# Optimization experiments

Measured on AMD Instinct MI355X. Metric: run time of the kernel, lower is better.

## Reference

```python
import jax, jax.numpy as jnp
import numpy as np

B = 64
D = 4096          # width of every layer
# DAG: layer k consumes concat of prior layer outputs listed here (0 = input x)
CONNECTIONS = {1: [0], 2: [0, 1], 3: [1, 2], 4: [2, 3]}


def setup_inputs() -> dict:
    key = jax.random.key(0)
    keys = iter(jax.random.split(key, 32))
    inp = {"x": jax.random.normal(next(keys), (B, D), dtype=jnp.float32)}
    for k, v in CONNECTIONS.items():
        fan_in = D * len(v)
        bound = 1.0 / np.sqrt(fan_in)
        # kaiming_uniform_(a=sqrt(5)) -> U(-sqrt(6/((1+5)*fan_in)), +) = U(-1/sqrt(fan_in), +)
        inp[f"W{k}"] = jax.random.uniform(next(keys), (D, fan_in), jnp.float32, -bound, bound)
        inp[f"b{k}"] = jax.random.uniform(next(keys), (D,), jnp.float32, -bound, bound)
        # static binary mask (buffer in torch), stored as float like MaskedLinear expects
        inp[f"M{k}"] = (jax.random.uniform(next(keys), (D, fan_in)) < 0.5).astype(jnp.float32)
    return inp


def _dag_forward(x, Ws, bs, Ms):
    layer_output = [x]
    for k, v in CONNECTIONS.items():
        inputs = jnp.concatenate([layer_output[v_] for v_ in v], axis=1)  # [B, D*len(v)]
        # masked linear: y = inputs @ (W*M)^T + b, then ReLU
        y = jnp.einsum('bi,oi->bo', inputs, Ws[k] * Ms[k]) + bs[k]
        layer_output.append(jax.nn.relu(y))
    return layer_output[-1]


def reference(x, W1, b1, M1, W2, b2, M2, W3, b3, M3, W4, b4, M4):
    Ws = {1: W1, 2: W2, 3: W3, 4: W4}
    bs = {1: b1, 2: b2, 3: b3, 4: b4}
    Ms = {1: M1, 2: M2, 3: M3, 4: M4}
    return _dag_forward(x, Ws, bs, Ms)
```

## Files before the change

kernel.cpp:

```cpp
#include <hip/hip_runtime.h>
#include <hip/hip_bf16.h>
#include <stdint.h>


typedef __attribute__((ext_vector_type(8))) short  s8v;
typedef __attribute__((ext_vector_type(4))) float  f4v;
typedef __attribute__((ext_vector_type(2))) float  f2v;
typedef __attribute__((ext_vector_type(4))) unsigned short us4v;
typedef __attribute__((ext_vector_type(2))) unsigned short us2v;

#define LDA 16384
#define MFMA16 __builtin_amdgcn_mfma_f32_16x16x32_bf16

__device__ __forceinline__ short f2bf(float f) {
  unsigned int u = __builtin_bit_cast(unsigned int, f);
  u += 0x7fffu + ((u >> 16) & 1u);
  return (short)(u >> 16);
}
__device__ __forceinline__ float bf2f(short s) {
  unsigned int u = ((unsigned int)(unsigned short)s) << 16;
  return __builtin_bit_cast(float, u);
}

__global__ void dag_splitx(const float* __restrict__ x,
                           ushort* __restrict__ xh, ushort* __restrict__ xl) {
  int idx = blockIdx.x * blockDim.x + threadIdx.x;
  int m = idx >> 10;
  int n = (idx & 1023) << 2;
  f4v v = *(const f4v*)(x + (size_t)m * 4096 + n);
  us4v h, l;
#pragma unroll
  for (int j = 0; j < 4; ++j) {
    short hh = f2bf(v[j]);
    h[j] = (unsigned short)hh;
    l[j] = (unsigned short)f2bf(v[j] - bf2f(hh));
  }
  *(us4v*)(xh + (size_t)m * LDA + n) = h;
  *(us4v*)(xl + (size_t)m * LDA + n) = l;
}

struct RA { s8v ah0, ah1, ah2, ah3, al0, al1, al2, al3; };

template <int NSUPER>
__global__ __launch_bounds__(256, 2) void dag_gemm_phaseA(
    const ushort* __restrict__ Ah,
    const ushort* __restrict__ Al,
    const float*  __restrict__ W,
    const float*  __restrict__ Mm,
    float*        __restrict__ partial,
    int K) {
  extern __shared__ float smem[];
  const int tid  = threadIdx.x;
  const int wave = tid >> 6, lane = tid & 63;
  const int l15  = lane & 15, blk = lane >> 4;
  const int n0   = blockIdx.x * 128 + wave * 32;
  const int klen = NSUPER * 64;
  const int kbeg = blockIdx.y * klen;

  float* WL = smem + wave * 4096;
  float* ML = WL + 2048;

  const int srow = lane >> 4;
  const int sc   = lane & 15;

  const ushort* ap  = Ah + (size_t)l15 * LDA + kbeg + blk * 8;
  const ushort* alp = Al + (size_t)l15 * LDA + kbeg + blk * 8;

  f4v stW[8], stM[8];
  f4v acc[4][2];
#pragma unroll
  for (int i = 0; i < 4; ++i) {
    acc[i][0] = (f4v){0.f, 0.f, 0.f, 0.f};
    acc[i][1] = (f4v){0.f, 0.f, 0.f, 0.f};
  }
  RA a0, a1;

  auto GLOAD = [&](int s) {
    const float* wb = W  + (size_t)n0 * K + kbeg + s * 64 + sc * 4;
    const float* mb = Mm + (size_t)n0 * K + kbeg + s * 64 + sc * 4;
#pragma unroll
    for (int j = 0; j < 8; ++j) {
      size_t ro = (size_t)(4 * j + srow) * K;
      stW[j] = *(const f4v*)(wb + ro);
      stM[j] = *(const f4v*)(mb + ro);
    }
  };
  auto DSWRITE = [&]() {
#pragma unroll
    for (int j = 0; j < 8; ++j) {
      int row = 4 * j + srow;
      int ci  = sc ^ (row & 15);
      *(f4v*)(WL + row * 64 + ci * 4) = stW[j];
      *(f4v*)(ML + row * 64 + ci * 4) = stM[j];
    }
  };
  auto LOADA = [&](RA& r, int ko) {
    r.ah0 = *(const s8v*)(ap  + ko);
    r.ah1 = *(const s8v*)(ap  + (size_t)16 * LDA + ko);
    r.ah2 = *(const s8v*)(ap  + (size_t)32 * LDA + ko);
    r.ah3 = *(const s8v*)(ap  + (size_t)48 * LDA + ko);
    r.al0 = *(const s8v*)(alp + ko);
    r.al1 = *(const s8v*)(alp + (size_t)16 * LDA + ko);
    r.al2 = *(const s8v*)(alp + (size_t)32 * LDA + ko);
    r.al3 = *(const s8v*)(alp + (size_t)48 * LDA + ko);
  };

  auto KSTEP = [&](int kstep, RA& ra) {
    const int cc = kstep * 8 + blk * 2;
    const int c0 = cc ^ l15, c1 = (cc + 1) ^ l15;
    const float* wr0 = WL + l15 * 64;
    const float* wr1 = WL + (l15 + 16) * 64;
    const float* mr0 = ML + l15 * 64;
    const float* mr1 = ML + (l15 + 16) * 64;
    f4v w0a = *(const f4v*)(wr0 + c0 * 4), w0b = *(const f4v*)(wr0 + c1 * 4);
    f4v w1a = *(const f4v*)(wr1 + c0 * 4), w1b = *(const f4v*)(wr1 + c1 * 4);
    f4v m0a = *(const f4v*)(mr0 + c0 * 4), m0b = *(const f4v*)(mr0 + c1 * 4);
    f4v m1a = *(const f4v*)(mr1 + c0 * 4), m1b = *(const f4v*)(mr1 + c1 * 4);

    s8v wh0, wl0, wh1, wl1;
#pragma unroll
    for (int j = 0; j < 4; ++j) {
      { float ww = w0a[j] * m0a[j]; short h = f2bf(ww);
        wh0[j]     = h; wl0[j]     = f2bf(ww - bf2f(h)); }
      { float ww = w0b[j] * m0b[j]; short h = f2bf(ww);
        wh0[j + 4] = h; wl0[j + 4] = f2bf(ww - bf2f(h)); }
      { float ww = w1a[j] * m1a[j]; short h = f2bf(ww);
        wh1[j]     = h; wl1[j]     = f2bf(ww - bf2f(h)); }
      { float ww = w1b[j] * m1b[j]; short h = f2bf(ww);
        wh1[j + 4] = h; wl1[j + 4] = f2bf(ww - bf2f(h)); }
    }
    acc[0][0] = MFMA16(ra.ah0, wh0, acc[0][0], 0, 0, 0);
    acc[0][0] = MFMA16(ra.al0, wh0, acc[0][0], 0, 0, 0);
    acc[0][0] = MFMA16(ra.ah0, wl0, acc[0][0], 0, 0, 0);
    acc[1][0] = MFMA16(ra.ah1, wh0, acc[1][0], 0, 0, 0);
    acc[1][0] = MFMA16(ra.al1, wh0, acc[1][0], 0, 0, 0);
    acc[1][0] = MFMA16(ra.ah1, wl0, acc[1][0], 0, 0, 0);
    acc[2][0] = MFMA16(ra.ah2, wh0, acc[2][0], 0, 0, 0);
    acc[2][0] = MFMA16(ra.al2, wh0, acc[2][0], 0, 0, 0);
    acc[2][0] = MFMA16(ra.ah2, wl0, acc[2][0], 0, 0, 0);
    acc[3][0] = MFMA16(ra.ah3, wh0, acc[3][0], 0, 0, 0);
    acc[3][0] = MFMA16(ra.al3, wh0, acc[3][0], 0, 0, 0);
    acc[3][0] = MFMA16(ra.ah3, wl0, acc[3][0], 0, 0, 0);
    acc[0][1] = MFMA16(ra.ah0, wh1, acc[0][1], 0, 0, 0);
    acc[0][1] = MFMA16(ra.al0, wh1, acc[0][1], 0, 0, 0);
    acc[0][1] = MFMA16(ra.ah0, wl1, acc[0][1], 0, 0, 0);
    acc[1][1] = MFMA16(ra.ah1, wh1, acc[1][1], 0, 0, 0);
    acc[1][1] = MFMA16(ra.al1, wh1, acc[1][1], 0, 0, 0);
    acc[1][1] = MFMA16(ra.ah1, wl1, acc[1][1], 0, 0, 0);
    acc[2][1] = MFMA16(ra.ah2, wh1, acc[2][1], 0, 0, 0);
    acc[2][1] = MFMA16(ra.al2, wh1, acc[2][1], 0, 0, 0);
    acc[2][1] = MFMA16(ra.ah2, wl1, acc[2][1], 0, 0, 0);
    acc[3][1] = MFMA16(ra.ah3, wh1, acc[3][1], 0, 0, 0);
    acc[3][1] = MFMA16(ra.al3, wh1, acc[3][1], 0, 0, 0);
    acc[3][1] = MFMA16(ra.ah3, wl1, acc[3][1], 0, 0, 0);
  };

  GLOAD(0);
  DSWRITE();
  if (NSUPER > 1) GLOAD(1);
  LOADA(a0, 0);
  LOADA(a1, 32);

#pragma unroll
  for (int s = 0; s < NSUPER; ++s) {
    KSTEP(0, a0);
    if (s + 1 < NSUPER) LOADA(a0, (s + 1) * 64);
    KSTEP(1, a1);
    if (s + 1 < NSUPER) LOADA(a1, (s + 1) * 64 + 32);
    if (s + 1 < NSUPER) {
      DSWRITE();
      if (s + 2 < NSUPER) GLOAD(s + 2);
    }
  }

  float* pout = partial + (size_t)blockIdx.y * (64 * 4096);
#pragma unroll
  for (int mt = 0; mt < 4; ++mt)
#pragma unroll
    for (int nt = 0; nt < 2; ++nt) {
      int n = n0 + nt * 16 + l15;
#pragma unroll
      for (int rr = 0; rr < 4; ++rr) {
        int m = mt * 16 + blk * 4 + rr;
        pout[(size_t)m * 4096 + n] = acc[mt][nt][rr];
      }
    }
}

__global__ void dag_phaseB(const float* __restrict__ partial, int splitk,
                           const float* __restrict__ bias,
                           ushort* __restrict__ yh, ushort* __restrict__ yl,
                           float* __restrict__ yf) {
  int idx = blockIdx.x * blockDim.x + threadIdx.x;
  int m = idx >> 11;
  int n = (idx & 2047) << 1;
  const float* p = partial + (size_t)m * 4096 + n;
  float s0 = 0.f, s1 = 0.f;
#pragma unroll 4
  for (int sp = 0; sp < splitk; ++sp) {
    f2v v = *(const f2v*)(p + (size_t)sp * (64 * 4096));
    s0 += v[0]; s1 += v[1];
  }
  const f2v bv = *(const f2v*)(bias + n);
  s0 = fmaxf(s0 + bv[0], 0.f);
  s1 = fmaxf(s1 + bv[1], 0.f);
  if (yf) {
    *(f2v*)(yf + (size_t)m * 4096 + n) = (f2v){s0, s1};
  } else {
    us2v h, l;
    short h0 = f2bf(s0); h[0] = (unsigned short)h0;
    l[0] = (unsigned short)f2bf(s0 - bf2f(h0));
    short h1 = f2bf(s1); h[1] = (unsigned short)h1;
    l[1] = (unsigned short)f2bf(s1 - bf2f(h1));
    *(us2v*)(yh + (size_t)m * LDA + n) = h;
    *(us2v*)(yl + (size_t)m * LDA + n) = l;
  }
}

extern "C" void kernel_launch(void* const* d_in, const int* in_sizes, int n_in,
                              void* d_out, int out_size, void* d_ws, size_t ws_size,
                              hipStream_t stream) {
  (void)in_sizes; (void)n_in; (void)out_size;
  const float* x = (const float*)d_in[0];
  struct L { const float *W, *b, *M; int K, incol, outcol; };
  L Ls[4] = {
      {(const float*)d_in[1],  (const float*)d_in[2],  (const float*)d_in[3],  4096, 0,    4096},
      {(const float*)d_in[4],  (const float*)d_in[5],  (const float*)d_in[6],  8192, 0,    8192},
      {(const float*)d_in[7],  (const float*)d_in[8],  (const float*)d_in[9],  8192, 4096, 12288},
      {(const float*)d_in[10], (const float*)d_in[11], (const float*)d_in[12], 8192, 8192, 16384},
  };
  float* out = (float*)d_out;

  char* ws = (char*)d_ws;
  ushort* Ah = (ushort*)ws;
  ushort* Al = (ushort*)(ws + (size_t)64 * LDA * 2);
  float* partial = (float*)(ws + (size_t)2 * 64 * LDA * 2);
  int SPLITK = 16;
  while (SPLITK > 4 &&
         ws_size < (size_t)4 * 1024 * 1024 + (size_t)SPLITK * 1024 * 1024)
    SPLITK >>= 1;

  dag_splitx<<<256, 256, 0, stream>>>(x, Ah, Al);

  const size_t smem = 65536;
  for (int k = 0; k < 4; ++k) {
    dim3 grid(32, SPLITK);
    const ushort* Ahp = Ah + Ls[k].incol;
    const ushort* Alp = Al + Ls[k].incol;
    int nsuper = (Ls[k].K / SPLITK) / 64;
    switch (nsuper) {
      case 4:
        dag_gemm_phaseA<4><<<grid, 256, smem, stream>>>(
            Ahp, Alp, Ls[k].W, Ls[k].M, partial, Ls[k].K);
        break;
      case 8:
        dag_gemm_phaseA<8><<<grid, 256, smem, stream>>>(
            Ahp, Alp, Ls[k].W, Ls[k].M, partial, Ls[k].K);
        break;
      default:
        dag_gemm_phaseA<16><<<grid, 256, smem, stream>>>(
            Ahp, Alp, Ls[k].W, Ls[k].M, partial, Ls[k].K);
        break;
    }
    bool last = (k == 3);
    dag_phaseB<<<512, 256, 0, stream>>>(
        partial, SPLITK, Ls[k].b,
        last ? (ushort*)nullptr : Ah + Ls[k].outcol,
        last ? (ushort*)nullptr : Al + Ls[k].outcol,
        last ? out : (float*)nullptr);
  }
}
```

Measured before the change: 280.9 us.

## Stream W and mask tiles directly into double-buffered LDS via global_load_lds

Replaces the register-staged global load plus LDS write of W and M tiles with direct global-to-LDS loads (global_load_lds), using two LDS buffers per wave so the next k-chunk is fetched while the current one is consumed. Waits are managed with explicit vmcnt counts and sched barriers. LDS per block doubles to 128 KB and launch bounds drop to one block per CU, which trades occupancy for fewer VGPRs and less staging traffic. The swizzle moves to the global source address. Correctness depends on the vmcnt accounting, and since each wave reads only its own LDS region, no block barrier is needed.

Result: faster. 268.8 us (-4.3%).

```diff
diff --git a/kernel.cpp b/kernel.cpp
--- a/kernel.cpp
+++ b/kernel.cpp
@@ -11,6 +11,9 @@
 
 #define LDA 16384
 #define MFMA16 __builtin_amdgcn_mfma_f32_16x16x32_bf16
+
+typedef __attribute__((address_space(3))) void       lds_void;
+typedef const __attribute__((address_space(1))) void g_void;
 
 __device__ __forceinline__ short f2bf(float f) {
   unsigned int u = __builtin_bit_cast(unsigned int, f);
@@ -42,7 +45,7 @@
 struct RA { s8v ah0, ah1, ah2, ah3, al0, al1, al2, al3; };
 
 template <int NSUPER>
-__global__ __launch_bounds__(256, 2) void dag_gemm_phaseA(
+__global__ __launch_bounds__(256, 1) void dag_gemm_phaseA(
     const ushort* __restrict__ Ah,
     const ushort* __restrict__ Al,
     const float*  __restrict__ W,
@@ -57,8 +60,11 @@
   const int klen = NSUPER * 64;
   const int kbeg = blockIdx.y * klen;
 
-  float* WL = smem + wave * 4096;
-  float* ML = WL + 2048;
+  float* base = smem + wave * 8192;
+  float* WL0 = base;
+  float* ML0 = base + 2048;
+  float* WL1 = base + 4096;
+  float* ML1 = base + 6144;
 
   const int srow = lane >> 4;
   const int sc   = lane & 15;
@@ -66,7 +72,6 @@
   const ushort* ap  = Ah + (size_t)l15 * LDA + kbeg + blk * 8;
   const ushort* alp = Al + (size_t)l15 * LDA + kbeg + blk * 8;
 
-  f4v stW[8], stM[8];
   f4v acc[4][2];
 #pragma unroll
   for (int i = 0; i < 4; ++i) {
@@ -75,23 +80,17 @@
   }
   RA a0, a1;
 
-  auto GLOAD = [&](int s) {
-    const float* wb = W  + (size_t)n0 * K + kbeg + s * 64 + sc * 4;
-    const float* mb = Mm + (size_t)n0 * K + kbeg + s * 64 + sc * 4;
+  auto GLDS = [&](int s, float* WB, float* MB) {
 #pragma unroll
     for (int j = 0; j < 8; ++j) {
-      size_t ro = (size_t)(4 * j + srow) * K;
-      stW[j] = *(const f4v*)(wb + ro);
-      stM[j] = *(const f4v*)(mb + ro);
-    }
-  };
-  auto DSWRITE = [&]() {
-#pragma unroll
-    for (int j = 0; j < 8; ++j) {
-      int row = 4 * j + srow;
-      int ci  = sc ^ (row & 15);
-      *(f4v*)(WL + row * 64 + ci * 4) = stW[j];
-      *(f4v*)(ML + row * 64 + ci * 4) = stM[j];
+      int row4 = 4 * j + srow;
+      int gc   = sc ^ (row4 & 15);
+      const float* ws = W  + (size_t)(n0 + row4) * K + kbeg + s * 64 + gc * 4;
+      const float* ms = Mm + (size_t)(n0 + row4) * K + kbeg + s * 64 + gc * 4;
+      __builtin_amdgcn_global_load_lds((g_void*)ws, (lds_void*)(WB + j * 256),
+                                       16, 0, 0);
+      __builtin_amdgcn_global_load_lds((g_void*)ms, (lds_void*)(MB + j * 256),
+                                       16, 0, 0);
     }
   };
   auto LOADA = [&](RA& r, int ko) {
@@ -105,7 +104,7 @@
     r.al3 = *(const s8v*)(alp + (size_t)48 * LDA + ko);
   };
 
-  auto KSTEP = [&](int kstep, RA& ra) {
+  auto KSTEP = [&](int kstep, RA& ra, float* WL, float* ML) {
     const int cc = kstep * 8 + blk * 2;
     const int c0 = cc ^ l15, c1 = (cc + 1) ^ l15;
     const float* wr0 = WL + l15 * 64;
@@ -155,21 +154,26 @@
     acc[3][1] = MFMA16(ra.ah3, wl1, acc[3][1], 0, 0, 0);
   };
 
-  GLOAD(0);
-  DSWRITE();
-  if (NSUPER > 1) GLOAD(1);
+  GLDS(0, WL0, ML0);
   LOADA(a0, 0);
   LOADA(a1, 32);
+  asm volatile("s_waitcnt vmcnt(16)" ::: "memory");
+  __builtin_amdgcn_sched_barrier(0);
 
 #pragma unroll
   for (int s = 0; s < NSUPER; ++s) {
-    KSTEP(0, a0);
+    float* curW = (s & 1) ? WL1 : WL0;
+    float* curM = (s & 1) ? ML1 : ML0;
+    float* nxtW = (s & 1) ? WL0 : WL1;
+    float* nxtM = (s & 1) ? ML0 : ML1;
+    if (s + 1 < NSUPER) GLDS(s + 1, nxtW, nxtM);
+    KSTEP(0, a0, curW, curM);
     if (s + 1 < NSUPER) LOADA(a0, (s + 1) * 64);
-    KSTEP(1, a1);
+    KSTEP(1, a1, curW, curM);
     if (s + 1 < NSUPER) LOADA(a1, (s + 1) * 64 + 32);
     if (s + 1 < NSUPER) {
-      DSWRITE();
-      if (s + 2 < NSUPER) GLOAD(s + 2);
+      asm volatile("s_waitcnt vmcnt(16)" ::: "memory");
+      __builtin_amdgcn_sched_barrier(0);
     }
   }
 
@@ -240,9 +244,16 @@
          ws_size < (size_t)4 * 1024 * 1024 + (size_t)SPLITK * 1024 * 1024)
     SPLITK >>= 1;
 
+  const int smem = 131072;
+  hipFuncSetAttribute((const void*)dag_gemm_phaseA<4>,
+                      hipFuncAttributeMaxDynamicSharedMemorySize, smem);
+  hipFuncSetAttribute((const void*)dag_gemm_phaseA<8>,
+                      hipFuncAttributeMaxDynamicSharedMemorySize, smem);
+  hipFuncSetAttribute((const void*)dag_gemm_phaseA<16>,
+                      hipFuncAttributeMaxDynamicSharedMemorySize, smem);
+
   dag_splitx<<<256, 256, 0, stream>>>(x, Ah, Al);
 
-  const size_t smem = 65536;
   for (int k = 0; k < 4; ++k) {
     dim3 grid(32, SPLITK);
     const ushort* Ahp = Ah + Ls[k].incol;
```
